# Performance work log

Measured on AMD Instinct MI355X. Metric: run time of the kernel, lower is better.

The kernel has to match this reference:

```python
import jax, jax.numpy as jnp
import numpy as np

N_NODES = 100000
N_EDGES = 600000
D = 128


def setup_inputs() -> dict:
    key = jax.random.key(0)
    ks = jax.random.split(key, 12)
    inp = {
        'feat': jax.random.normal(ks[0], (N_NODES, D), dtype=jnp.float32),
        'W_tran': jax.random.normal(ks[1], (D, D), dtype=jnp.float32) * (1.0 / np.sqrt(D)),
        'att_w1': jax.random.normal(ks[2], (4 * D, D), dtype=jnp.float32) * (1.0 / np.sqrt(D)),
        'att_b1': jax.random.normal(ks[3], (4 * D,), dtype=jnp.float32) * 0.01,
        'att_w2': jax.random.normal(ks[4], (1, 4 * D), dtype=jnp.float32) * (1.0 / np.sqrt(4 * D)),
        'trans_w': jax.random.uniform(ks[5], (N_EDGES,), dtype=jnp.float32),
        'geo_src': jax.random.randint(ks[6], (N_EDGES,), 0, N_NODES, dtype=jnp.int32),
        'geo_dst': jax.random.randint(ks[7], (N_EDGES,), 0, N_NODES, dtype=jnp.int32),
        'cat_src': jax.random.randint(ks[8], (N_EDGES,), 0, N_NODES, dtype=jnp.int32),
        'cat_dst': jax.random.randint(ks[9], (N_EDGES,), 0, N_NODES, dtype=jnp.int32),
        'trans_src': jax.random.randint(ks[10], (N_EDGES,), 0, N_NODES, dtype=jnp.int32),
        'trans_dst': jax.random.randint(ks[11], (N_EDGES,), 0, N_NODES, dtype=jnp.int32),
    }
    return inp


def _mean_agg(f, src, dst, n):
    # copy_u('f','m') then mean('m', .) : gather src feats, segment-mean by dst
    msum = jax.ops.segment_sum(f[src], dst, num_segments=n)
    cnt = jax.ops.segment_sum(jnp.ones((src.shape[0],), f.dtype), dst, num_segments=n)
    return msum / jnp.maximum(cnt, 1.0)[:, None]


def reference(feat, W_tran, att_w1, att_b1, att_w2, trans_w,
              geo_src, geo_dst, cat_src, cat_dst, trans_src, trans_dst):
    n = feat.shape[0]
    # feat_tran: Linear(D, D, bias=False) -> x @ W^T
    f = feat @ W_tran.T
    geo = _mean_agg(f, geo_src, geo_dst, n)            # [N, D]
    cat = _mean_agg(f, cat_src, cat_dst, n)            # [N, D]
    # u_mul_e('f','w') then sum: weighted gather + segment-sum by dst
    trans = jax.ops.segment_sum(f[trans_src] * trans_w[:, None], trans_dst, num_segments=n)
    z = jnp.stack([geo, trans, cat], axis=1)           # [N, 3, D]
    # SemanticAttention: Linear -> tanh -> Linear(no bias), mean over nodes, softmax over relations
    h = jnp.tanh(jnp.einsum('nrd,hd->nrh', z, att_w1) + att_b1)   # [N, 3, 4D]
    w = jnp.einsum('nrh,oh->nro', h, att_w2).mean(0)              # [3, 1]
    beta = jax.nn.softmax(w, axis=0)                              # [3, 1]
    fused = (beta[None, :, :] * z).sum(1)                         # [N, D]
    return jax.nn.leaky_relu(fused, negative_slope=0.2)
```

## Files before the change

kernel.cpp:

```cpp
#include <hip/hip_runtime.h>
#include <math.h>

#define DD 128
#define NNODES 100000
#define NEDGES 600000
#define NREL 3
#define MTOT (NREL*NNODES)
#define NTILES (NNODES/16)
#define RT_PER_BLK 8
#define NBLK_REL ((NTILES + RT_PER_BLK - 1)/RT_PER_BLK)
#define ATT_WAVES 8

#define BSHIFT 9
#define NBUCK ((NNODES + 511) >> BSHIFT)
#define GBUCK (NREL*NBUCK)
#define CAP 4096
#define P1_THREADS 512
#define P1_EPT 8
#define P1_EPB (P1_THREADS*P1_EPT)
#define P1_BLOCKS ((NREL*NEDGES + P1_EPB - 1)/P1_EPB)

#define TR_BLOCKS ((NTILES + 7)/8)
#define CVT_BLOCKS ((512*DD/4 + 511)/512)
#define FRONT_BLOCKS (P1_BLOCKS + TR_BLOCKS + CVT_BLOCKS)

#define AGGU_BLOCKS ((2*NNODES*16)/256)
#define AGGW_BLOCKS ((NNODES*16)/256)

typedef __attribute__((ext_vector_type(8))) short short8;
typedef __attribute__((ext_vector_type(4))) float f32x4;

__device__ inline float bf2f(unsigned short u){ return __uint_as_float(((unsigned int)u)<<16); }
__device__ inline float bflo(unsigned int u){ return __uint_as_float(u<<16); }
__device__ inline float bfhi(unsigned int u){ return __uint_as_float(u & 0xffff0000u); }
__device__ inline unsigned short f2bf(float f){
    unsigned int i = __float_as_uint(f);
    unsigned int r = (i + 0x7fffu + ((i>>16)&1u)) >> 16;
    return (unsigned short)r;
}
__device__ inline unsigned int pack2(float lo, float hi){
    return (unsigned int)f2bf(lo) | ((unsigned int)f2bf(hi) << 16);
}
__device__ inline short8 cvt8(const float* __restrict__ p){
    f32x4 a = *(const f32x4*)p;
    f32x4 b = *(const f32x4*)(p+4);
    short8 t;
    t[0]=(short)f2bf(a[0]); t[1]=(short)f2bf(a[1]); t[2]=(short)f2bf(a[2]); t[3]=(short)f2bf(a[3]);
    t[4]=(short)f2bf(b[0]); t[5]=(short)f2bf(b[1]); t[6]=(short)f2bf(b[2]); t[7]=(short)f2bf(b[3]);
    return t;
}
__device__ inline void acc8(float* a, float w, uint4 v){
    a[0] += w*bflo(v.x); a[1] += w*bfhi(v.x);
    a[2] += w*bflo(v.y); a[3] += w*bfhi(v.y);
    a[4] += w*bflo(v.z); a[5] += w*bfhi(v.z);
    a[6] += w*bflo(v.w); a[7] += w*bfhi(v.w);
}

__global__ __launch_bounds__(512) void k_front(
    const float* __restrict__ feat, const float* __restrict__ W,
    const float* __restrict__ aw1,
    const int* __restrict__ s0, const int* __restrict__ d0,
    const int* __restrict__ s1, const int* __restrict__ d1,
    const int* __restrict__ s2, const int* __restrict__ d2,
    const float* __restrict__ tw,
    int* __restrict__ bcur, int2* __restrict__ slab, float* __restrict__ wslab,
    unsigned short* __restrict__ w1_bf, unsigned short* __restrict__ f_out)
{
    __shared__ int hist[GBUCK];
    int bid = blockIdx.x;

    if (bid < P1_BLOCKS){
        for (int i=threadIdx.x; i<GBUCK; i+=512) hist[i]=0;
        __syncthreads();

        int e0 = bid * P1_EPB;
        int ss[P1_EPT], dd_[P1_EPT], gb[P1_EPT]; float wv[P1_EPT];
        #pragma unroll
        for (int j=0;j<P1_EPT;++j){
            int e = e0 + j*512 + threadIdx.x;
            gb[j] = -1;
            if (e < NREL*NEDGES){
                int rel = e / NEDGES; int i = e - rel*NEDGES;
                const int* s = (rel==0)?s0:(rel==1)?s1:s2;
                const int* d = (rel==0)?d0:(rel==1)?d1:d2;
                ss[j]=s[i]; dd_[j]=d[i];
                wv[j] = (rel==2)? tw[i] : 0.f;
                gb[j] = rel*NBUCK + (dd_[j]>>BSHIFT);
                atomicAdd(&hist[gb[j]], 1);
            }
        }
        __syncthreads();
        for (int i=threadIdx.x; i<GBUCK; i+=512){
            int c = hist[i];
            hist[i] = (c>0) ? atomicAdd(&bcur[i], c) : 0;
        }
        __syncthreads();
        #pragma unroll
        for (int j=0;j<P1_EPT;++j){
            if (gb[j] >= 0){
                int off = atomicAdd(&hist[gb[j]], 1);
                int2 pr; pr.x = ss[j]; pr.y = dd_[j];
                slab[(size_t)gb[j]*CAP + off] = pr;
                if (gb[j] >= 2*NBUCK) wslab[(size_t)(gb[j]-2*NBUCK)*CAP + off] = wv[j];
            }
        }
    } else if (bid < P1_BLOCKS + TR_BLOCKS){
        int wid = (bid - P1_BLOCKS)*8 + (threadIdx.x>>6);
        if (wid >= NTILES) return;
        int lane = threadIdx.x & 63;
        int m = lane & 15, quad = lane >> 4;
        int n0 = wid*16;

        short8 a[4];
        const float* arow = feat + (size_t)(n0+m)*DD;
        #pragma unroll
        for (int ks=0; ks<4; ++ks) a[ks] = cvt8(arow + ks*32 + quad*8);

        #pragma unroll
        for (int ct=0; ct<8; ++ct){
            f32x4 acc = {0.f,0.f,0.f,0.f};
            const float* brow = W + (size_t)(ct*16+m)*DD;
            #pragma unroll
            for (int ks=0; ks<4; ++ks){
                short8 b = cvt8(brow + ks*32 + quad*8);
                acc = __builtin_amdgcn_mfma_f32_16x16x32_bf16(a[ks], b, acc, 0,0,0);
            }
            int col = ct*16 + m;
            #pragma unroll
            for (int i=0;i<4;++i)
                f_out[(size_t)(n0+quad*4+i)*DD + col] = f2bf(acc[i]);
        }
    } else {
        int gid = (bid - P1_BLOCKS - TR_BLOCKS)*512 + threadIdx.x;
        if (gid < 512*DD/4){
            f32x4 v = ((const f32x4*)aw1)[gid];
            ushort4 o;
            o.x=f2bf(v[0]); o.y=f2bf(v[1]); o.z=f2bf(v[2]); o.w=f2bf(v[3]);
            ((ushort4*)w1_bf)[gid] = o;
        }
    }
}

__global__ __launch_bounds__(512) void k_csr(
    const int2* __restrict__ slab, const float* __restrict__ wslab,
    const int* __restrict__ bcur,
    int* __restrict__ offs, int* __restrict__ cnt,
    int* __restrict__ es, float* __restrict__ ewt)
{
    __shared__ int lcnt[512];
    __shared__ int lsc[512];
    __shared__ int psum[512];
    int gb = blockIdx.x;
    int rel = gb / NBUCK, b = gb - rel*NBUCK;
    int n0 = b << BSHIFT;
    int nn = min(512, NNODES - n0);
    int ecount = bcur[gb];
    const int2* ep = slab + (size_t)gb*CAP;
    int t = threadIdx.x;

    int acc = (t < gb) ? bcur[t] : 0;
    if (t + 512 < gb) acc += bcur[t + 512];
    psum[t] = acc; __syncthreads();
    for (int off=256; off; off>>=1){
        if (t < off) psum[t] += psum[t+off];
        __syncthreads();
    }
    int base = psum[0];
    __syncthreads();

    lcnt[t] = 0; __syncthreads();
    for (int i=t; i<ecount; i+=512)
        atomicAdd(&lcnt[ep[i].y - n0], 1);
    __syncthreads();
    int v = lcnt[t];
    psum[t] = v; __syncthreads();
    for (int off=1; off<512; off<<=1){
        int x = (t>=off)? psum[t-off] : 0;
        __syncthreads(); psum[t] += x; __syncthreads();
    }
    int ex = (t>0)? psum[t-1] : 0;
    lsc[t] = ex;
    __syncthreads();
    if (t < nn){
        offs[rel*NNODES + n0 + t] = base + ex;
        cnt [rel*NNODES + n0 + t] = v;
    }
    for (int i=t; i<ecount; i+=512){
        int2 pr = ep[i];
        int pos = base + atomicAdd(&lsc[pr.y - n0], 1);
        es[pos] = pr.x;
        if (rel==2) ewt[pos - 2*NEDGES] = wslab[(size_t)b*CAP + i];
    }
}

__global__ __launch_bounds__(256) void k_agg(
    const unsigned short* __restrict__ f,
    const int* __restrict__ es, const float* __restrict__ ewt,
    const int* __restrict__ offs, const int* __restrict__ cnt,
    unsigned short* __restrict__ z)
{
    int bid = blockIdx.x;
    if (bid < AGGU_BLOCKS){
        int gid = bid*256 + threadIdx.x;
        int g = gid >> 4;
        int c = gid & 15;
        int start = offs[g];
        int deg   = cnt[g];
        float a[8] = {0,0,0,0,0,0,0,0};
        int i = 0;
        for (; i+3 < deg; i += 4){
            int s0 = es[start+i],   s1 = es[start+i+1];
            int s2 = es[start+i+2], s3 = es[start+i+3];
            uint4 v0 = *(const uint4*)(f + (size_t)s0*DD + c*8);
            uint4 v1 = *(const uint4*)(f + (size_t)s1*DD + c*8);
            uint4 v2 = *(const uint4*)(f + (size_t)s2*DD + c*8);
            uint4 v3 = *(const uint4*)(f + (size_t)s3*DD + c*8);
            acc8(a, 1.f, v0); acc8(a, 1.f, v1); acc8(a, 1.f, v2); acc8(a, 1.f, v3);
        }
        if (i+1 < deg){
            int s0 = es[start+i], s1 = es[start+i+1];
            uint4 v0 = *(const uint4*)(f + (size_t)s0*DD + c*8);
            uint4 v1 = *(const uint4*)(f + (size_t)s1*DD + c*8);
            acc8(a, 1.f, v0); acc8(a, 1.f, v1);
            i += 2;
        }
        if (i < deg){
            int s = es[start+i];
            uint4 v = *(const uint4*)(f + (size_t)s*DD + c*8);
            acc8(a, 1.f, v);
        }
        float sc = 1.f/fmaxf((float)deg, 1.f);
        uint4 o;
        o.x = pack2(a[0]*sc, a[1]*sc);
        o.y = pack2(a[2]*sc, a[3]*sc);
        o.z = pack2(a[4]*sc, a[5]*sc);
        o.w = pack2(a[6]*sc, a[7]*sc);
        *(uint4*)(z + (size_t)g*DD + c*8) = o;
    } else {
        int gid = (bid - AGGU_BLOCKS)*256 + threadIdx.x;
        int g = (gid >> 4) + 2*NNODES;
        int c = gid & 15;
        int start = offs[g];
        int deg   = cnt[g];
        float a[8] = {0,0,0,0,0,0,0,0};
        int i = 0;
        for (; i+3 < deg; i += 4){
            int s0 = es[start+i],   s1 = es[start+i+1];
            int s2 = es[start+i+2], s3 = es[start+i+3];
            float w0 = ewt[start+i   - 2*NEDGES];
            float w1 = ewt[start+i+1 - 2*NEDGES];
            float w2 = ewt[start+i+2 - 2*NEDGES];
            float w3 = ewt[start+i+3 - 2*NEDGES];
            uint4 v0 = *(const uint4*)(f + (size_t)s0*DD + c*8);
            uint4 v1 = *(const uint4*)(f + (size_t)s1*DD + c*8);
            uint4 v2 = *(const uint4*)(f + (size_t)s2*DD + c*8);
            uint4 v3 = *(const uint4*)(f + (size_t)s3*DD + c*8);
            acc8(a, w0, v0); acc8(a, w1, v1); acc8(a, w2, v2); acc8(a, w3, v3);
        }
        if (i+1 < deg){
            int s0 = es[start+i], s1 = es[start+i+1];
            float w0 = ewt[start+i   - 2*NEDGES];
            float w1 = ewt[start+i+1 - 2*NEDGES];
            uint4 v0 = *(const uint4*)(f + (size_t)s0*DD + c*8);
            uint4 v1 = *(const uint4*)(f + (size_t)s1*DD + c*8);
            acc8(a, w0, v0); acc8(a, w1, v1);
            i += 2;
        }
        if (i < deg){
            int s = es[start+i];
            float w = ewt[start+i - 2*NEDGES];
            uint4 v = *(const uint4*)(f + (size_t)s*DD + c*8);
            acc8(a, w, v);
        }
        uint4 o;
        o.x = pack2(a[0], a[1]);
        o.y = pack2(a[2], a[3]);
        o.z = pack2(a[4], a[5]);
        o.w = pack2(a[6], a[7]);
        *(uint4*)(z + (size_t)g*DD + c*8) = o;
    }
}

__global__ __launch_bounds__(512, 4) void k_att(
    const unsigned short* __restrict__ z,
    const unsigned short* __restrict__ w1,
    const float* __restrict__ bias1,
    const float* __restrict__ wv2,
    float* __restrict__ w_part)
{
    __shared__ uint4 sm[RT_PER_BLK*256];
    __shared__ float sred[ATT_WAVES];
    const float C2 = 2.8853900817779268f;

    int rel = blockIdx.x / NBLK_REL;
    int nb  = blockIdx.x % NBLK_REL;
    int trt0 = nb * RT_PER_BLK;
    int rt_count = min(RT_PER_BLK, NTILES - trt0);
    int row0 = trt0 * 16;
    const unsigned short* zrel = z + (size_t)rel*NNODES*DD;

    int lane = threadIdx.x & 63;
    int wv   = threadIdx.x >> 6;
    int m = lane & 15, quad = lane >> 4;

    short8 bq[16];
    float ww[4], bbc[4];
    #pragma unroll
    for (int ct=0; ct<4; ++ct){
        int col = (wv*4 + ct)*16 + m;
        const short8* brow = (const short8*)(w1 + (size_t)col*DD);
        #pragma unroll
        for (int ks=0; ks<4; ++ks) bq[ct*4+ks] = brow[ks*4 + quad];
        ww[ct]  = wv2[col];
        bbc[ct] = bias1[col] * C2;
    }

    int valid_rows = rt_count * 16;
    #pragma unroll
    for (int i=0; i<4; ++i){
        int u = i*512 + threadIdx.x;
        int row = u >> 4, kc = u & 15;
        if (row < valid_rows){
            uint4 v = *(const uint4*)(zrel + (size_t)(row0+row)*DD + kc*8);
            int rt = row >> 4, mm = row & 15;
            sm[rt*256 + kc*16 + (mm ^ kc)] = v;
        }
    }
    __syncthreads();

    const short8* smx = (const short8*)sm;
    int o0 = (0  + quad)*16 + (m ^ (0  + quad));
    int o1 = (4  + quad)*16 + (m ^ (4  + quad));
    int o2 = (8  + quad)*16 + (m ^ (8  + quad));
    int o3 = (12 + quad)*16 + (m ^ (12 + quad));

    float s_r[4] = {0.f,0.f,0.f,0.f};
    short8 a0 = smx[o0], a1 = smx[o1], a2 = smx[o2], a3 = smx[o3];
    for (int rt=0; rt<rt_count; ++rt){
        short8 n0_, n1_, n2_, n3_;
        if (rt+1 < rt_count){
            int nbse = (rt+1)*256;
            n0_ = smx[nbse + o0];
            n1_ = smx[nbse + o1];
            n2_ = smx[nbse + o2];
            n3_ = smx[nbse + o3];
        } else { n0_ = a0; n1_ = a1; n2_ = a2; n3_ = a3; }
        #pragma unroll
        for (int ct=0; ct<4; ++ct){
            f32x4 acc = {0.f,0.f,0.f,0.f};
            acc = __builtin_amdgcn_mfma_f32_16x16x32_bf16(a0, bq[ct*4+0], acc, 0,0,0);
            acc = __builtin_amdgcn_mfma_f32_16x16x32_bf16(a1, bq[ct*4+1], acc, 0,0,0);
            acc = __builtin_amdgcn_mfma_f32_16x16x32_bf16(a2, bq[ct*4+2], acc, 0,0,0);
            acc = __builtin_amdgcn_mfma_f32_16x16x32_bf16(a3, bq[ct*4+3], acc, 0,0,0);
            #pragma unroll
            for (int i=0;i<4;++i){
                float e = __builtin_amdgcn_exp2f(__builtin_fmaf(acc[i], C2, bbc[ct]));
                s_r[ct] += __builtin_amdgcn_rcpf(e + 1.f);
            }
        }
        a0 = n0_; a1 = n1_; a2 = n2_; a3 = n3_;
    }
    float s_all = 0.f;
    #pragma unroll
    for (int ct=0; ct<4; ++ct)
        s_all += ww[ct]*(float)(4*rt_count) - 2.f*ww[ct]*s_r[ct];
    #pragma unroll
    for (int off=32; off; off>>=1) s_all += __shfl_xor(s_all, off);
    if (lane == 0) sred[wv] = s_all;
    __syncthreads();
    if (threadIdx.x == 0){
        float tt = 0.f;
        #pragma unroll
        for (int i=0;i<ATT_WAVES;++i) tt += sred[i];
        atomicAdd(&w_part[rel*8 + (nb & 7)], tt);
    }
}

__global__ __launch_bounds__(256) void k_final(
    const unsigned short* __restrict__ z0, const unsigned short* __restrict__ z1,
    const unsigned short* __restrict__ z2,
    const float* __restrict__ w_part, float* __restrict__ out)
{
    int gid = blockIdx.x*256 + threadIdx.x;
    if (gid >= NNODES*DD/4) return;
    const float invN = 1.f / (float)NNODES;
    float w0=0.f, w1=0.f, w2=0.f;
    #pragma unroll
    for (int i=0;i<8;++i){ w0 += w_part[i]; w1 += w_part[8+i]; w2 += w_part[16+i]; }
    w0 *= invN; w1 *= invN; w2 *= invN;
    float mx = fmaxf(w0, fmaxf(w1, w2));
    const float LOG2E = 1.4426950408889634f;
    float e0 = __builtin_amdgcn_exp2f((w0-mx)*LOG2E);
    float e1 = __builtin_amdgcn_exp2f((w1-mx)*LOG2E);
    float e2 = __builtin_amdgcn_exp2f((w2-mx)*LOG2E);
    float inv = 1.f/(e0+e1+e2);
    float b0 = e0*inv, b1 = e1*inv, b2 = e2*inv;
    ushort4 g = ((const ushort4*)z0)[gid];
    ushort4 t = ((const ushort4*)z1)[gid];
    ushort4 c = ((const ushort4*)z2)[gid];
    f32x4 o;
    float gv[4] = {bf2f(g.x),bf2f(g.y),bf2f(g.z),bf2f(g.w)};
    float tv[4] = {bf2f(t.x),bf2f(t.y),bf2f(t.z),bf2f(t.w)};
    float cv[4] = {bf2f(c.x),bf2f(c.y),bf2f(c.z),bf2f(c.w)};
    #pragma unroll
    for (int i=0;i<4;++i){
        float x = b0*gv[i] + b1*tv[i] + b2*cv[i];
        o[i] = (x > 0.f) ? x : 0.2f*x;
    }
    ((f32x4*)out)[gid] = o;
}

extern "C" void kernel_launch(void* const* d_in, const int* in_sizes, int n_in,
                              void* d_out, int out_size, void* d_ws, size_t ws_size,
                              hipStream_t stream)
{
    const float* feat = (const float*)d_in[0];
    const float* W    = (const float*)d_in[1];
    const float* aw1  = (const float*)d_in[2];
    const float* ab1  = (const float*)d_in[3];
    const float* aw2  = (const float*)d_in[4];
    const float* tw   = (const float*)d_in[5];
    const int* geo_src   = (const int*)d_in[6];
    const int* geo_dst   = (const int*)d_in[7];
    const int* cat_src   = (const int*)d_in[8];
    const int* cat_dst   = (const int*)d_in[9];
    const int* trans_src = (const int*)d_in[10];
    const int* trans_dst = (const int*)d_in[11];

    char* ws = (char*)d_ws;
    float* w_part = (float*)ws;
    int*   bcur   = (int*)(w_part + 64);
    int*   offs   = bcur + 640;
    int*   cnt    = offs + MTOT;
    unsigned short* w1_bf = (unsigned short*)(cnt + MTOT);
    int*   es     = (int*)(w1_bf + 512*DD);
    float* ewt    = (float*)(es + NREL*NEDGES);
    unsigned short* z = (unsigned short*)(ewt + NEDGES);
    int2*  slab   = (int2*)z;
    float* wslab  = (float*)(slab + (size_t)GBUCK*CAP);
    unsigned short* f_bf = (unsigned short*)d_out;

    (void)hipMemsetAsync(w_part, 0, (64 + 640)*sizeof(int), stream);

    k_front<<<FRONT_BLOCKS, 512, 0, stream>>>(feat, W, aw1,
                                              geo_src, geo_dst, cat_src, cat_dst,
                                              trans_src, trans_dst, tw,
                                              bcur, slab, wslab, w1_bf, f_bf);

    k_csr<<<GBUCK, 512, 0, stream>>>(slab, wslab, bcur, offs, cnt, es, ewt);

    k_agg<<<AGGU_BLOCKS + AGGW_BLOCKS, 256, 0, stream>>>(f_bf, es, ewt, offs, cnt, z);

    k_att<<<NREL*NBLK_REL, 512, 0, stream>>>(z, w1_bf, ab1, aw2, w_part);

    unsigned short* z_geo   = z;
    unsigned short* z_cat   = z + (size_t)NNODES*DD;
    unsigned short* z_trans = z + (size_t)2*NNODES*DD;
    int dg = (NNODES*DD/4 + 255)/256;
    k_final<<<dg, 256, 0, stream>>>(z_geo, z_cat, z_trans, w_part, (float*)d_out);
}
```

Baseline: 357.6 us.

## Fuse CSR build and neighbor aggregation into one kernel using LDS edge lists

Result: no change. 357.5 us (-0.0%).

```diff
diff --git a/kernel.cpp b/kernel.cpp
--- a/kernel.cpp
+++ b/kernel.cpp
@@ -15,6 +15,7 @@
 #define NBUCK ((NNODES + 511) >> BSHIFT)
 #define GBUCK (NREL*NBUCK)
 #define CAP 4096
+#define CAPH 2048
 #define P1_THREADS 512
 #define P1_EPT 8
 #define P1_EPB (P1_THREADS*P1_EPT)
@@ -23,9 +24,6 @@
 #define TR_BLOCKS ((NTILES + 7)/8)
 #define CVT_BLOCKS ((512*DD/4 + 511)/512)
 #define FRONT_BLOCKS (P1_BLOCKS + TR_BLOCKS + CVT_BLOCKS)
-
-#define AGGU_BLOCKS ((2*NNODES*16)/256)
-#define AGGW_BLOCKS ((NNODES*16)/256)
 
 typedef __attribute__((ext_vector_type(8))) short short8;
 typedef __attribute__((ext_vector_type(4))) float f32x4;
@@ -141,143 +139,127 @@
     }
 }
 
-__global__ __launch_bounds__(512) void k_csr(
+__global__ __launch_bounds__(512) void k_csragg(
     const int2* __restrict__ slab, const float* __restrict__ wslab,
     const int* __restrict__ bcur,
-    int* __restrict__ offs, int* __restrict__ cnt,
-    int* __restrict__ es, float* __restrict__ ewt)
+    const unsigned short* __restrict__ f,
+    unsigned short* __restrict__ z)
 {
-    __shared__ int lcnt[512];
-    __shared__ int lsc[512];
-    __shared__ int psum[512];
-    int gb = blockIdx.x;
-    int rel = gb / NBUCK, b = gb - rel*NBUCK;
-    int n0 = b << BSHIFT;
-    int nn = min(512, NNODES - n0);
+    __shared__ int lcnt[256];
+    __shared__ int lsc[256];
+    __shared__ int psum[256];
+    __shared__ int es_l[CAPH];
+    __shared__ float ewt_l[CAPH];
+
+    int gb2 = blockIdx.x;
+    int rel = gb2 / (2*NBUCK);
+    int rem = gb2 - rel*2*NBUCK;
+    int b = rem >> 1, half = rem & 1;
+    int hn0 = (b << BSHIFT) + half*256;
+    if (hn0 >= NNODES) return;
+    int nn = min(256, NNODES - hn0);
+    int gb = rel*NBUCK + b;
     int ecount = bcur[gb];
     const int2* ep = slab + (size_t)gb*CAP;
     int t = threadIdx.x;
-
-    int acc = (t < gb) ? bcur[t] : 0;
-    if (t + 512 < gb) acc += bcur[t + 512];
-    psum[t] = acc; __syncthreads();
-    for (int off=256; off; off>>=1){
-        if (t < off) psum[t] += psum[t+off];
+    bool wr = (rel == 2);
+
+    if (t < 256) lcnt[t] = 0;
+    __syncthreads();
+    for (int i=t; i<ecount; i+=512){
+        unsigned lo = (unsigned)(ep[i].y - hn0);
+        if (lo < 256u) atomicAdd(&lcnt[lo], 1);
+    }
+    __syncthreads();
+    int v = 0;
+    if (t < 256){ v = lcnt[t]; psum[t] = v; }
+    __syncthreads();
+    for (int off=1; off<256; off<<=1){
+        int x = 0;
+        if (t < 256 && t >= off) x = psum[t-off];
         __syncthreads();
-    }
-    int base = psum[0];
-    __syncthreads();
-
-    lcnt[t] = 0; __syncthreads();
-    for (int i=t; i<ecount; i+=512)
-        atomicAdd(&lcnt[ep[i].y - n0], 1);
-    __syncthreads();
-    int v = lcnt[t];
-    psum[t] = v; __syncthreads();
-    for (int off=1; off<512; off<<=1){
-        int x = (t>=off)? psum[t-off] : 0;
-        __syncthreads(); psum[t] += x; __syncthreads();
-    }
-    int ex = (t>0)? psum[t-1] : 0;
-    lsc[t] = ex;
-    __syncthreads();
-    if (t < nn){
-        offs[rel*NNODES + n0 + t] = base + ex;
-        cnt [rel*NNODES + n0 + t] = v;
-    }
+        if (t < 256) psum[t] += x;
+        __syncthreads();
+    }
+    if (t < 256) lsc[t] = psum[t] - v;
+    __syncthreads();
     for (int i=t; i<ecount; i+=512){
         int2 pr = ep[i];
-        int pos = base + atomicAdd(&lsc[pr.y - n0], 1);
-        es[pos] = pr.x;
-        if (rel==2) ewt[pos - 2*NEDGES] = wslab[(size_t)b*CAP + i];
-    }
-}
-
-__global__ __launch_bounds__(256) void k_agg(
-    const unsigned short* __restrict__ f,
-    const int* __restrict__ es, const float* __restrict__ ewt,
-    const int* __restrict__ offs, const int* __restrict__ cnt,
-    unsigned short* __restrict__ z)
-{
-    int bid = blockIdx.x;
-    if (bid < AGGU_BLOCKS){
-        int gid = bid*256 + threadIdx.x;
-        int g = gid >> 4;
-        int c = gid & 15;
-        int start = offs[g];
-        int deg   = cnt[g];
+        unsigned lo = (unsigned)(pr.y - hn0);
+        if (lo < 256u){
+            int pos = atomicAdd(&lsc[lo], 1);
+            es_l[pos] = pr.x;
+            if (wr) ewt_l[pos] = wslab[(size_t)b*CAP + i];
+        }
+    }
+    __syncthreads();
+
+    int grp = t >> 4, c = t & 15;
+    for (int pass=0; pass<8; ++pass){
+        int n = pass*32 + grp;
+        if (n >= nn) break;
+        int deg = lcnt[n];
+        int start = lsc[n] - deg;
         float a[8] = {0,0,0,0,0,0,0,0};
         int i = 0;
-        for (; i+3 < deg; i += 4){
-            int s0 = es[start+i],   s1 = es[start+i+1];
-            int s2 = es[start+i+2], s3 = es[start+i+3];
-            uint4 v0 = *(const uint4*)(f + (size_t)s0*DD + c*8);
-            uint4 v1 = *(const uint4*)(f + (size_t)s1*DD + c*8);
-            uint4 v2 = *(const uint4*)(f + (size_t)s2*DD + c*8);
-            uint4 v3 = *(const uint4*)(f + (size_t)s3*DD + c*8);
-            acc8(a, 1.f, v0); acc8(a, 1.f, v1); acc8(a, 1.f, v2); acc8(a, 1.f, v3);
-        }
-        if (i+1 < deg){
-            int s0 = es[start+i], s1 = es[start+i+1];
-            uint4 v0 = *(const uint4*)(f + (size_t)s0*DD + c*8);
-            uint4 v1 = *(const uint4*)(f + (size_t)s1*DD + c*8);
-            acc8(a, 1.f, v0); acc8(a, 1.f, v1);
-            i += 2;
-        }
-        if (i < deg){
-            int s = es[start+i];
-            uint4 v = *(const uint4*)(f + (size_t)s*DD + c*8);
-            acc8(a, 1.f, v);
-        }
-        float sc = 1.f/fmaxf((float)deg, 1.f);
-        uint4 o;
-        o.x = pack2(a[0]*sc, a[1]*sc);
-        o.y = pack2(a[2]*sc, a[3]*sc);
-        o.z = pack2(a[4]*sc, a[5]*sc);
-        o.w = pack2(a[6]*sc, a[7]*sc);
-        *(uint4*)(z + (size_t)g*DD + c*8) = o;
-    } else {
-        int gid = (bid - AGGU_BLOCKS)*256 + threadIdx.x;
-        int g = (gid >> 4) + 2*NNODES;
-        int c = gid & 15;
-        int start = offs[g];
-        int deg   = cnt[g];
-        float a[8] = {0,0,0,0,0,0,0,0};
-        int i = 0;
-        for (; i+3 < deg; i += 4){
-            int s0 = es[start+i],   s1 = es[start+i+1];
-            int s2 = es[start+i+2], s3 = es[start+i+3];
-            float w0 = ewt[start+i   - 2*NEDGES];
-            float w1 = ewt[start+i+1 - 2*NEDGES];
-            float w2 = ewt[start+i+2 - 2*NEDGES];
-            float w3 = ewt[start+i+3 - 2*NEDGES];
-            uint4 v0 = *(const uint4*)(f + (size_t)s0*DD + c*8);
-            uint4 v1 = *(const uint4*)(f + (size_t)s1*DD + c*8);
-            uint4 v2 = *(const uint4*)(f + (size_t)s2*DD + c*8);
-            uint4 v3 = *(const uint4*)(f + (size_t)s3*DD + c*8);
-            acc8(a, w0, v0); acc8(a, w1, v1); acc8(a, w2, v2); acc8(a, w3, v3);
-        }
-        if (i+1 < deg){
-            int s0 = es[start+i], s1 = es[start+i+1];
-            float w0 = ewt[start+i   - 2*NEDGES];
-            float w1 = ewt[start+i+1 - 2*NEDGES];
-            uint4 v0 = *(const uint4*)(f + (size_t)s0*DD + c*8);
-            uint4 v1 = *(const uint4*)(f + (size_t)s1*DD + c*8);
-            acc8(a, w0, v0); acc8(a, w1, v1);
-            i += 2;
-        }
-        if (i < deg){
-            int s = es[start+i];
-            float w = ewt[start+i - 2*NEDGES];
-            uint4 v = *(const uint4*)(f + (size_t)s*DD + c*8);
-            acc8(a, w, v);
+        if (!wr){
+            for (; i+3 < deg; i += 4){
+                int s0 = es_l[start+i],   s1 = es_l[start+i+1];
+                int s2 = es_l[start+i+2], s3 = es_l[start+i+3];
+                uint4 v0 = *(const uint4*)(f + (size_t)s0*DD + c*8);
+                uint4 v1 = *(const uint4*)(f + (size_t)s1*DD + c*8);
+                uint4 v2 = *(const uint4*)(f + (size_t)s2*DD + c*8);
+                uint4 v3 = *(const uint4*)(f + (size_t)s3*DD + c*8);
+                acc8(a,1.f,v0); acc8(a,1.f,v1); acc8(a,1.f,v2); acc8(a,1.f,v3);
+            }
+            if (i+1 < deg){
+                int s0 = es_l[start+i], s1 = es_l[start+i+1];
+                uint4 v0 = *(const uint4*)(f + (size_t)s0*DD + c*8);
+                uint4 v1 = *(const uint4*)(f + (size_t)s1*DD + c*8);
+                acc8(a,1.f,v0); acc8(a,1.f,v1);
+                i += 2;
+            }
+            if (i < deg){
+                int s = es_l[start+i];
+                uint4 vv = *(const uint4*)(f + (size_t)s*DD + c*8);
+                acc8(a,1.f,vv);
+            }
+            float sc = 1.f/fmaxf((float)deg, 1.f);
+            #pragma unroll
+            for (int k=0;k<8;++k) a[k] *= sc;
+        } else {
+            for (; i+3 < deg; i += 4){
+                int s0 = es_l[start+i],   s1 = es_l[start+i+1];
+                int s2 = es_l[start+i+2], s3 = es_l[start+i+3];
+                float w0 = ewt_l[start+i],   w1 = ewt_l[start+i+1];
+                float w2 = ewt_l[start+i+2], w3 = ewt_l[start+i+3];
+                uint4 v0 = *(const uint4*)(f + (size_t)s0*DD + c*8);
+                uint4 v1 = *(const uint4*)(f + (size_t)s1*DD + c*8);
+                uint4 v2 = *(const uint4*)(f + (size_t)s2*DD + c*8);
+                uint4 v3 = *(const uint4*)(f + (size_t)s3*DD + c*8);
+                acc8(a,w0,v0); acc8(a,w1,v1); acc8(a,w2,v2); acc8(a,w3,v3);
+            }
+            if (i+1 < deg){
+                int s0 = es_l[start+i], s1 = es_l[start+i+1];
+                float w0 = ewt_l[start+i], w1 = ewt_l[start+i+1];
+                uint4 v0 = *(const uint4*)(f + (size_t)s0*DD + c*8);
+                uint4 v1 = *(const uint4*)(f + (size_t)s1*DD + c*8);
+                acc8(a,w0,v0); acc8(a,w1,v1);
+                i += 2;
+            }
+            if (i < deg){
+                int s = es_l[start+i];
+                float w = ewt_l[start+i];
+                uint4 vv = *(const uint4*)(f + (size_t)s*DD + c*8);
+                acc8(a,w,vv);
+            }
         }
         uint4 o;
         o.x = pack2(a[0], a[1]);
         o.y = pack2(a[2], a[3]);
         o.z = pack2(a[4], a[5]);
         o.w = pack2(a[6], a[7]);
-        *(uint4*)(z + (size_t)g*DD + c*8) = o;
+        *(uint4*)(z + (size_t)(rel*NNODES + hn0 + n)*DD + c*8) = o;
     }
 }
 
@@ -430,15 +412,12 @@
     char* ws = (char*)d_ws;
     float* w_part = (float*)ws;
     int*   bcur   = (int*)(w_part + 64);
-    int*   offs   = bcur + 640;
-    int*   cnt    = offs + MTOT;
-    unsigned short* w1_bf = (unsigned short*)(cnt + MTOT);
-    int*   es     = (int*)(w1_bf + 512*DD);
-    float* ewt    = (float*)(es + NREL*NEDGES);
-    unsigned short* z = (unsigned short*)(ewt + NEDGES);
-    int2*  slab   = (int2*)z;
-    float* wslab  = (float*)(slab + (size_t)GBUCK*CAP);
+    unsigned short* w1_bf = (unsigned short*)(bcur + 640);
+    unsigned short* z = w1_bf + 512*DD;
+
     unsigned short* f_bf = (unsigned short*)d_out;
+    int2*  slab  = (int2*)((char*)d_out + (size_t)NNODES*DD*sizeof(unsigned short));
+    float* wslab = (float*)(slab + (size_t)GBUCK*CAP);
 
     (void)hipMemsetAsync(w_part, 0, (64 + 640)*sizeof(int), stream);
 
@@ -447,9 +426,7 @@
                                               trans_src, trans_dst, tw,
                                               bcur, slab, wslab, w1_bf, f_bf);
 
-    k_csr<<<GBUCK, 512, 0, stream>>>(slab, wslab, bcur, offs, cnt, es, ewt);
-
-    k_agg<<<AGGU_BLOCKS + AGGW_BLOCKS, 256, 0, stream>>>(f_bf, es, ewt, offs, cnt, z);
+    k_csragg<<<NREL*2*NBUCK, 512, 0, stream>>>(slab, wslab, bcur, f_bf, z);
 
     k_att<<<NREL*NBLK_REL, 512, 0, stream>>>(z, w1_bf, ab1, aw2, w_part);
 
```
